# Performance work log

Measured on AMD Instinct MI355X. Metric: run time of the kernel, lower is better.

Reference implementation:

```python
import jax, jax.numpy as jnp
import numpy as np

BN_EPS = 1e-5

# Binary_a: sign forward, hard-tanh STE backward (grad zeroed where |x| >= 1)
@jax.custom_vjp
def binary_act(x):
    return jnp.sign(x)

def _ba_fwd(x):
    return jnp.sign(x), x

def _ba_bwd(x, g):
    return (jnp.where((x > -1.0) & (x < 1.0), g, 0.0),)

binary_act.defvjp(_ba_fwd, _ba_bwd)

# Binary_w: sign forward, identity STE backward
@jax.custom_vjp
def binary_w(x):
    return jnp.sign(x)

def _bw_fwd(x):
    return jnp.sign(x), None

def _bw_bwd(_, g):
    return (g,)

binary_w.defvjp(_bw_fwd, _bw_bwd)


def setup_inputs() -> dict:
    key = jax.random.key(0)
    k1, k2, k3 = jax.random.split(key, 3)
    B, Cin, Cout, H, Wd, K = 32, 256, 256, 56, 56, 3
    x = jax.random.normal(k1, (B, Cin, H, Wd), dtype=jnp.float32)
    weight = jax.random.normal(k2, (Cout, Cin, K, K), dtype=jnp.float32) * 0.05
    bias = jax.random.normal(k3, (Cout,), dtype=jnp.float32) * 0.01
    gamma = jnp.ones((Cout,), dtype=jnp.float32)
    beta = jnp.zeros((Cout,), dtype=jnp.float32)
    return {"x": x, "weight": weight, "bias": bias, "gamma": gamma, "beta": beta}


def reference(x, weight, bias, gamma, beta):
    # activation binarization (A=2)
    xb = binary_act(x)
    # weight quantization (W=2): mean-center over in-channel dim, clamp to [-1,1]
    # (done on .data in torch -> values change but no grad through this step)
    wc_val = jnp.clip(weight - jnp.mean(weight, axis=1, keepdims=True), -1.0, 1.0)
    wc = weight + jax.lax.stop_gradient(wc_val - weight)
    # per-output-filter scale alpha = E[|w|] over (in, kh, kw)
    alpha = jnp.mean(jnp.abs(wc), axis=(1, 2, 3), keepdims=True)
    wq = binary_w(wc) * alpha  # [O,I,K,K]
    # conv2d, stride 1, padding 1, groups 1
    y = jax.lax.conv_general_dilated(
        xb, wq, window_strides=(1, 1), padding=((1, 1), (1, 1)),
        dimension_numbers=("NCHW", "OIHW", "NCHW"))
    y = y + bias[None, :, None, None]
    # BatchNorm2d, training-mode forward (biased batch stats)
    mean = jnp.mean(y, axis=(0, 2, 3), keepdims=True)
    var = jnp.mean(jnp.square(y - mean), axis=(0, 2, 3), keepdims=True)
    y = (y - mean) * jax.lax.rsqrt(var + BN_EPS)
    y = y * gamma[None, :, None, None] + beta[None, :, None, None]
    # last_relu=1
    return jax.nn.relu(y)
```

## Files before the change

kernel.cpp:

```cpp
#include <hip/hip_runtime.h>
#include <stdint.h>

typedef unsigned long long u64;
typedef unsigned int u32;

#define B_    32
#define CIN   256
#define COUT  256
#define H_    56
#define W_    56
#define HW    3136
#define NPOS  100352
#define NROW  1792
#define NPACKBLK 784


__global__ __launch_bounds__(256) void k_prep(
    const float* __restrict__ x,
    const float* __restrict__ wgt,
    u64* __restrict__ xbits,
    u64* __restrict__ wbits,
    float* __restrict__ alpha,
    int* __restrict__ ssum,
    unsigned long long* __restrict__ qsum)
{
    const int tid = threadIdx.x;

    if (blockIdx.x < NPACKBLK) {
        const int j = blockIdx.x / 196;
        const int p2 = (blockIdx.x - j * 196) * 256 + tid;
        const int pos0 = p2 * 2;
        const int b = pos0 / HW;
        const int hw = pos0 - b * HW;
        const float* xp = x + (size_t)b * CIN * HW + (size_t)j * 64 * HW + hw;
        u64 b0 = 0, b1 = 0;
#pragma unroll 8
        for (int k = 0; k < 64; ++k) {
            const float2 v = *(const float2*)(xp + (size_t)k * HW);
            b0 |= (u64)(v.x > 0.0f) << k;
            b1 |= (u64)(v.y > 0.0f) << k;
        }
        xbits[(size_t)pos0 * 4 + j] = b0;
        xbits[(size_t)(pos0 + 1) * 4 + j] = b1;
        return;
    }

    const int o = blockIdx.x - NPACKBLK;
    const int i = tid;
    const int wave = i >> 6, lane = i & 63;
    __shared__ float sred[4][12];

    if (i == 0) { ssum[o] = 0; qsum[o] = 0ULL; }

    float w9[9];
#pragma unroll
    for (int t = 0; t < 9; ++t) w9[t] = wgt[(o * 256 + i) * 9 + t];

    float m[9];
#pragma unroll
    for (int t = 0; t < 9; ++t) m[t] = w9[t];
#pragma unroll
    for (int s = 1; s < 64; s <<= 1)
#pragma unroll
        for (int t = 0; t < 9; ++t) m[t] += __shfl_xor(m[t], s, 64);
    if (lane == 0) {
#pragma unroll
        for (int t = 0; t < 9; ++t) sred[wave][t] = m[t];
    }
    __syncthreads();
#pragma unroll
    for (int t = 0; t < 9; ++t)
        m[t] = (sred[0][t] + sred[1][t] + sred[2][t] + sred[3][t]) * (1.0f / 256.0f);

    float wc[9];
    float asum = 0.0f;
#pragma unroll
    for (int t = 0; t < 9; ++t) {
        float v = w9[t] - m[t];
        v = fminf(fmaxf(v, -1.0f), 1.0f);
        wc[t] = v;
        asum += fabsf(v);
    }
#pragma unroll
    for (int s = 1; s < 64; s <<= 1) asum += __shfl_xor(asum, s, 64);
    __syncthreads();
    if (lane == 0) sred[wave][9] = asum;
    __syncthreads();
    if (i == 0)
        alpha[o] = (sred[0][9] + sred[1][9] + sred[2][9] + sred[3][9]) * (1.0f / 2304.0f);

#pragma unroll
    for (int t = 0; t < 9; ++t) {
        u64 bb = __ballot(wc[t] > 0.0f);
        if (lane == 0) wbits[o * 36 + t * 4 + wave] = bb;
    }
}

template<int R0, int R1>
__device__ __forceinline__ void run_row2(
    const u64* __restrict__ t2,
    const u64* wr,
    short* __restrict__ srow,
    const bool st,
    int& s_acc, int& q_acc)
{
    constexpr int NR = R1 - R0 + 1;
    u64 xc[4][NR][2];

#define FILL(col, slot) { \
    _Pragma("unroll") \
    for (int r = 0; r < NR; ++r) { \
        const ulonglong2 v = *(const ulonglong2*)&t2[((R0 + r) * 56 + (col)) * 4]; \
        xc[slot][r][0] = v.x; xc[slot][r][1] = v.y; } }

#define PIN(slot) { \
    _Pragma("unroll") \
    for (int r = 0; r < NR; ++r) { \
        asm volatile("" : "+v"(xc[slot][r][0])); \
        asm volatile("" : "+v"(xc[slot][r][1])); } }

#define TAPACC(slot, r, kw) \
    acc += (int)__popcll(xc[slot][r][0] ^ wr[((R0 + r) * 3 + (kw)) * 2 + 0]) \
         + (int)__popcll(xc[slot][r][1] ^ wr[((R0 + r) * 3 + (kw)) * 2 + 1]);

#define COMPW(sm, s0, sp, SROWOFF) { \
    int acc = 0; \
    _Pragma("unroll") \
    for (int r = 0; r < NR; ++r) { TAPACC(sm, r, 0) TAPACC(s0, r, 1) TAPACC(sp, r, 2) } \
    acc += __shfl_xor(acc, 1, 64); \
    const int Sv = NR * 3 * 256 - 2 * acc; \
    if (st) srow[(SROWOFF) * 256] = (short)Sv; \
    s_acc += Sv; q_acc += Sv * Sv; }

    FILL(0, 0) FILL(1, 1) FILL(2, 2) PIN(0) PIN(1)

    {
        int acc = 0;
#pragma unroll
        for (int r = 0; r < NR; ++r) { TAPACC(0, r, 1) TAPACC(1, r, 2) }
        acc += __shfl_xor(acc, 1, 64);
        const int Sv = NR * 2 * 256 - 2 * acc;
        if (st) srow[0] = (short)Sv;
        s_acc += Sv; q_acc += Sv * Sv;
    }
    FILL(3, 3) PIN(2)

    COMPW(0, 1, 2, 1) PIN(3)

    for (int wb = 2; wb <= 50; wb += 4) {
        FILL(wb + 2, 0) COMPW(1, 2, 3, wb + 0) PIN(0)
        FILL(wb + 3, 1) COMPW(2, 3, 0, wb + 1) PIN(1)
        FILL(wb + 4, 2) COMPW(3, 0, 1, wb + 2) PIN(2)
        FILL(wb + 5, 3) COMPW(0, 1, 2, wb + 3) PIN(3)
    }

    COMPW(1, 2, 3, 54)

    {
        int acc = 0;
#pragma unroll
        for (int r = 0; r < NR; ++r) { TAPACC(2, r, 0) TAPACC(3, r, 1) }
        acc += __shfl_xor(acc, 1, 64);
        const int Sv = NR * 2 * 256 - 2 * acc;
        if (st) srow[55 * 256] = (short)Sv;
        s_acc += Sv; q_acc += Sv * Sv;
    }

#undef FILL
#undef PIN
#undef TAPACC
#undef COMPW
}

__global__ __launch_bounds__(256, 4) void kc_conv(
    const u64* __restrict__ xbits,
    const u64* __restrict__ wbits,
    short* __restrict__ S,
    int* __restrict__ ssum,
    unsigned long long* __restrict__ qsum)
{
    const int blk = blockIdx.x;
    const int row = blk >> 1;
    const int ohalf = blk & 1;
    const int b = row / H_;
    const int h = row - b * H_;
    const int t = threadIdx.x;
    const int half = t & 1;
    const int o = ohalf * 128 + (t >> 1);

    __shared__ u64 tile[3 * W_ * 4];
    for (int idx = t; idx < 3 * W_ * 4; idx += 256) {
        int r = idx / (W_ * 4);
        int rem = idx - r * (W_ * 4);
        int hr = min(max(h - 1 + r, 0), H_ - 1);
        tile[idx] = xbits[((size_t)(b * HW + hr * W_)) * 4 + rem];
    }

    u64 wr[18];
#pragma unroll
    for (int tap = 0; tap < 9; ++tap) {
        ulonglong2 v = *(const ulonglong2*)(wbits + (size_t)o * 36 + tap * 4 + 2 * half);
        wr[tap * 2] = v.x;
        wr[tap * 2 + 1] = v.y;
    }
#pragma unroll
    for (int i = 0; i < 18; ++i) asm volatile("" : "+v"(wr[i]));

    __syncthreads();

    const u64* t2 = tile + 2 * half;
    short* srow = S + ((size_t)(b * HW + h * W_)) * 256 + o;
    int s_acc = 0, q_acc = 0;
    const bool st = (half == 0);
    if (h == 0)        run_row2<1, 2>(t2, wr, srow, st, s_acc, q_acc);
    else if (h == 55)  run_row2<0, 1>(t2, wr, srow, st, s_acc, q_acc);
    else               run_row2<0, 2>(t2, wr, srow, st, s_acc, q_acc);

    if (st) {
        atomicAdd(&ssum[o], s_acc);
        atomicAdd(&qsum[o], (unsigned long long)(long long)q_acc);
    }
}

__global__ __launch_bounds__(256) void kb_apply(
    const short* __restrict__ S,
    const int* __restrict__ ssum,
    const unsigned long long* __restrict__ qsum,
    const float* __restrict__ alpha,
    const float* __restrict__ gamma,
    const float* __restrict__ beta,
    float* __restrict__ out)
{
    const int blk = blockIdx.x;
    const int ps = blk % 7;
    const int bcg = blk / 7;
    const int cg = bcg & 3;
    const int b = bcg >> 2;
    const int c0 = cg * 64;
    const int pbase = ps * 448;
    const int tid = threadIdx.x;

    __shared__ float s_scale[64], s_shift[64];
    __shared__ u32 lds[64 * 33];

    if (tid < 64) {
        const int o = c0 + tid;
        const double N = (double)NPOS;
        double meanS = (double)ssum[o] / N;
        double varS = (double)qsum[o] / N - meanS * meanS;
        double a = (double)alpha[o];
        double rstd = 1.0 / sqrt(a * a * varS + 1e-5);
        double g = (double)gamma[o];
        s_scale[tid] = (float)(g * a * rstd);
        s_shift[tid] = (float)((double)beta[o] - g * a * meanS * rstd);
    }
    __syncthreads();

    for (int chunk = 0; chunk < 7; ++chunk) {
        const int p0 = pbase + chunk * 64;

        const u32* Sp = (const u32*)(S + ((size_t)b * HW + p0) * 256 + c0);
#pragma unroll
        for (int k = 0; k < 8; ++k) {
            const int idx = tid + k * 256;
            const int p = idx >> 5, cp = idx & 31;
            lds[p * 33 + cp] = Sp[p * 128 + cp];
        }
        __syncthreads();

        const int pl = tid & 63;
        const int ch4 = tid >> 6;
        const short* lss = (const short*)lds;
#pragma unroll
        for (int cc = 0; cc < 16; ++cc) {
            const int c = ch4 * 16 + cc;
            const float f = fmaxf(fmaf((float)lss[pl * 66 + c], s_scale[c], s_shift[c]), 0.0f);
            out[((size_t)(b * COUT + c0 + c)) * HW + p0 + pl] = f;
        }
        __syncthreads();
    }
}

extern "C" void kernel_launch(void* const* d_in, const int* in_sizes, int n_in,
                              void* d_out, int out_size, void* d_ws, size_t ws_size,
                              hipStream_t stream) {
    const float* x     = (const float*)d_in[0];
    const float* wgt   = (const float*)d_in[1];
    const float* gamma = (const float*)d_in[3];
    const float* beta  = (const float*)d_in[4];
    float* out = (float*)d_out;

    char* ws = (char*)d_ws;
    u64*   wbits = (u64*)(ws + 0);
    float* alpha = (float*)(ws + 73728);
    int*   ssum  = (int*)(ws + 74752);
    unsigned long long* qsum = (unsigned long long*)(ws + 75776);
    u64*   xbits = (u64*)(ws + 79872);
    short* Sarr  = (short*)(ws + 3291136);

    k_prep<<<NPACKBLK + 256, 256, 0, stream>>>(x, wgt, xbits, wbits, alpha, ssum, qsum);
    kc_conv<<<2 * NROW, 256, 0, stream>>>(xbits, wbits, Sarr, ssum, qsum);
    kb_apply<<<32 * 4 * 7, 256, 0, stream>>>(Sarr, ssum, qsum, alpha, gamma, beta, out);
}
```

Before: 330.2 us.

## Replace XNOR-popcount conv with int8 MFMA implicit GEMM on ±1 values

The binary convolution no longer uses XOR/popcount on packed bit words. Activation bits are expanded to ±1 int8 values in a swizzled LDS tile (zero where padded), and weights are pre-laid out as ±1 int8 MFMA B fragments. Each block then computes one output row against all 256 output channels with v_mfma_i32_32x32x32_i8, software-pipelining the operand loads. This trades popcount ALU work for matrix-core throughput, at the cost of 8x more operand bytes, extra LDS expansion work, and lower occupancy (launch bounds 3).

```diff
diff --git a/kernel.cpp b/kernel.cpp
--- a/kernel.cpp
+++ b/kernel.cpp
@@ -3,6 +3,8 @@
 
 typedef unsigned long long u64;
 typedef unsigned int u32;
+typedef int v4i __attribute__((ext_vector_type(4)));
+typedef int v16i __attribute__((ext_vector_type(16)));
 
 #define B_    32
 #define CIN   256
@@ -19,7 +21,7 @@
     const float* __restrict__ x,
     const float* __restrict__ wgt,
     u64* __restrict__ xbits,
-    u64* __restrict__ wbits,
+    int8_t* __restrict__ Bfrag,
     float* __restrict__ alpha,
     int* __restrict__ ssum,
     unsigned long long* __restrict__ qsum)
@@ -91,134 +93,129 @@
 
 #pragma unroll
     for (int t = 0; t < 9; ++t) {
-        u64 bb = __ballot(wc[t] > 0.0f);
-        if (lane == 0) wbits[o * 36 + t * 4 + wave] = bb;
+        const int8_t sv = (wc[t] > 0.0f) ? (int8_t)1 : (int8_t)-1;
+        const size_t addr =
+            ((size_t)((t * 8 + (i >> 5)) * 8 + (o >> 5)) * 64
+             + (size_t)(((i >> 4) & 1) * 32 + (o & 31))) * 16 + (i & 15);
+        Bfrag[addr] = sv;
     }
 }
 
-template<int R0, int R1>
-__device__ __forceinline__ void run_row2(
-    const u64* __restrict__ t2,
-    const u64* wr,
-    short* __restrict__ srow,
-    const bool st,
-    int& s_acc, int& q_acc)
-{
-    constexpr int NR = R1 - R0 + 1;
-    u64 xc[4][NR][2];
-
-#define FILL(col, slot) { \
-    _Pragma("unroll") \
-    for (int r = 0; r < NR; ++r) { \
-        const ulonglong2 v = *(const ulonglong2*)&t2[((R0 + r) * 56 + (col)) * 4]; \
-        xc[slot][r][0] = v.x; xc[slot][r][1] = v.y; } }
-
-#define PIN(slot) { \
-    _Pragma("unroll") \
-    for (int r = 0; r < NR; ++r) { \
-        asm volatile("" : "+v"(xc[slot][r][0])); \
-        asm volatile("" : "+v"(xc[slot][r][1])); } }
-
-#define TAPACC(slot, r, kw) \
-    acc += (int)__popcll(xc[slot][r][0] ^ wr[((R0 + r) * 3 + (kw)) * 2 + 0]) \
-         + (int)__popcll(xc[slot][r][1] ^ wr[((R0 + r) * 3 + (kw)) * 2 + 1]);
-
-#define COMPW(sm, s0, sp, SROWOFF) { \
-    int acc = 0; \
-    _Pragma("unroll") \
-    for (int r = 0; r < NR; ++r) { TAPACC(sm, r, 0) TAPACC(s0, r, 1) TAPACC(sp, r, 2) } \
-    acc += __shfl_xor(acc, 1, 64); \
-    const int Sv = NR * 3 * 256 - 2 * acc; \
-    if (st) srow[(SROWOFF) * 256] = (short)Sv; \
-    s_acc += Sv; q_acc += Sv * Sv; }
-
-    FILL(0, 0) FILL(1, 1) FILL(2, 2) PIN(0) PIN(1)
-
-    {
-        int acc = 0;
-#pragma unroll
-        for (int r = 0; r < NR; ++r) { TAPACC(0, r, 1) TAPACC(1, r, 2) }
-        acc += __shfl_xor(acc, 1, 64);
-        const int Sv = NR * 2 * 256 - 2 * acc;
-        if (st) srow[0] = (short)Sv;
-        s_acc += Sv; q_acc += Sv * Sv;
-    }
-    FILL(3, 3) PIN(2)
-
-    COMPW(0, 1, 2, 1) PIN(3)
-
-    for (int wb = 2; wb <= 50; wb += 4) {
-        FILL(wb + 2, 0) COMPW(1, 2, 3, wb + 0) PIN(0)
-        FILL(wb + 3, 1) COMPW(2, 3, 0, wb + 1) PIN(1)
-        FILL(wb + 4, 2) COMPW(3, 0, 1, wb + 2) PIN(2)
-        FILL(wb + 5, 3) COMPW(0, 1, 2, wb + 3) PIN(3)
-    }
-
-    COMPW(1, 2, 3, 54)
-
-    {
-        int acc = 0;
-#pragma unroll
-        for (int r = 0; r < NR; ++r) { TAPACC(2, r, 0) TAPACC(3, r, 1) }
-        acc += __shfl_xor(acc, 1, 64);
-        const int Sv = NR * 2 * 256 - 2 * acc;
-        if (st) srow[55 * 256] = (short)Sv;
-        s_acc += Sv; q_acc += Sv * Sv;
-    }
-
-#undef FILL
-#undef PIN
-#undef TAPACC
-#undef COMPW
-}
-
-__global__ __launch_bounds__(256, 4) void kc_conv(
+#define MFMA_I8(acc, a, b) \
+    asm volatile("v_mfma_i32_32x32x32_i8 %0, %1, %2, %0" : "+a"(acc) : "v"(a), "v"(b))
+
+__global__ __launch_bounds__(256, 3) void kc_mfma(
     const u64* __restrict__ xbits,
-    const u64* __restrict__ wbits,
+    const int8_t* __restrict__ Bfrag,
     short* __restrict__ S,
     int* __restrict__ ssum,
     unsigned long long* __restrict__ qsum)
 {
     const int blk = blockIdx.x;
-    const int row = blk >> 1;
-    const int ohalf = blk & 1;
-    const int b = row / H_;
-    const int h = row - b * H_;
-    const int t = threadIdx.x;
-    const int half = t & 1;
-    const int o = ohalf * 128 + (t >> 1);
-
-    __shared__ u64 tile[3 * W_ * 4];
-    for (int idx = t; idx < 3 * W_ * 4; idx += 256) {
-        int r = idx / (W_ * 4);
-        int rem = idx - r * (W_ * 4);
-        int hr = min(max(h - 1 + r, 0), H_ - 1);
-        tile[idx] = xbits[((size_t)(b * HW + hr * W_)) * 4 + rem];
-    }
-
-    u64 wr[18];
-#pragma unroll
-    for (int tap = 0; tap < 9; ++tap) {
-        ulonglong2 v = *(const ulonglong2*)(wbits + (size_t)o * 36 + tap * 4 + 2 * half);
-        wr[tap * 2] = v.x;
-        wr[tap * 2 + 1] = v.y;
-    }
-#pragma unroll
-    for (int i = 0; i < 18; ++i) asm volatile("" : "+v"(wr[i]));
-
-    __syncthreads();
-
-    const u64* t2 = tile + 2 * half;
-    short* srow = S + ((size_t)(b * HW + h * W_)) * 256 + o;
-    int s_acc = 0, q_acc = 0;
-    const bool st = (half == 0);
-    if (h == 0)        run_row2<1, 2>(t2, wr, srow, st, s_acc, q_acc);
-    else if (h == 55)  run_row2<0, 1>(t2, wr, srow, st, s_acc, q_acc);
-    else               run_row2<0, 2>(t2, wr, srow, st, s_acc, q_acc);
-
-    if (st) {
-        atomicAdd(&ssum[o], s_acc);
-        atomicAdd(&qsum[o], (unsigned long long)(long long)q_acc);
+    const int b = blk / H_;
+    const int h = blk - b * H_;
+    const int tid = threadIdx.x;
+
+    __shared__ u32 ldsb[3 * 66 * 64];
+
+    for (int it = tid; it < 3 * 58 * 16; it += 256) {
+        const int r = it / 928;
+        const int rem = it - r * 928;
+        const int wp = rem >> 4;
+        const int g = rem & 15;
+        const int hr = h - 1 + r;
+        const int w_in = wp - 1;
+        const bool inb = (hr >= 0) && (hr < H_) && (w_in >= 0) && (w_in < W_);
+        u32 chunk16 = 0;
+        if (inb) {
+            const u64 word = xbits[((size_t)(b * HW + hr * W_ + w_in)) * 4 + (g >> 2)];
+            chunk16 = (u32)(word >> ((g & 3) * 16)) & 0xFFFFu;
+        }
+        u32 out4[4];
+#pragma unroll
+        for (int d = 0; d < 4; ++d) {
+            const u32 nib = (chunk16 >> (4 * d)) & 0xFu;
+            const u32 m1 = (nib * 0x00204081u) & 0x01010101u;
+            const u32 inv = m1 ^ 0x01010101u;
+            out4[d] = inb ? (0x01010101u ^ (inv * 0xFEu)) : 0u;
+        }
+        const int gs = (g + wp) & 15;
+        u32* dst = &ldsb[((r * 66 + wp) << 6) + gs * 4];
+        dst[0] = out4[0]; dst[1] = out4[1]; dst[2] = out4[2]; dst[3] = out4[3];
+    }
+    __syncthreads();
+
+    const int m0 = tid & 31;
+    const int lh = (tid >> 5) & 1;
+    const int wv = tid >> 6;
+    const int8_t* smem = (const int8_t*)ldsb;
+    const int8_t* Bp = Bfrag + (size_t)(tid & 63) * 16;
+
+    auto ldA = [&](int kk, int mt) -> v4i {
+        const int tap = kk >> 3, s = kk & 7;
+        const int dh = tap / 3;
+        const int dw = tap - dh * 3;
+        const int wpm = mt * 32 + m0 + dw;
+        const int gs = (2 * s + lh + wpm) & 15;
+        const int addr = ((dh * 66 + wpm) << 8) + (gs << 4);
+        return *(const v4i*)(smem + addr);
+    };
+    auto ldB = [&](int kk, int ntl) -> v4i {
+        const size_t off = (size_t)((kk * 8) + wv * 2 + ntl) * 1024;
+        return *(const v4i*)(Bp + off);
+    };
+
+    v16i acc00 = {0}, acc01 = {0}, acc10 = {0}, acc11 = {0};
+
+    v4i a0 = ldA(0, 0), a1 = ldA(0, 1);
+    v4i b0 = ldB(0, 0), b1 = ldB(0, 1);
+    v4i a0n, a1n, b0n, b1n;
+
+    for (int kk = 0; kk < 72; kk += 2) {
+        a0n = ldA(kk + 1, 0); a1n = ldA(kk + 1, 1);
+        b0n = ldB(kk + 1, 0); b1n = ldB(kk + 1, 1);
+        MFMA_I8(acc00, a0, b0); MFMA_I8(acc01, a0, b1);
+        MFMA_I8(acc10, a1, b0); MFMA_I8(acc11, a1, b1);
+        if (kk + 2 < 72) {
+            a0 = ldA(kk + 2, 0); a1 = ldA(kk + 2, 1);
+            b0 = ldB(kk + 2, 0); b1 = ldB(kk + 2, 1);
+        }
+        MFMA_I8(acc00, a0n, b0n); MFMA_I8(acc01, a0n, b1n);
+        MFMA_I8(acc10, a1n, b0n); MFMA_I8(acc11, a1n, b1n);
+    }
+
+    asm volatile("s_nop 7\n\ts_nop 7\n\ts_nop 7"
+                 : "+a"(acc00), "+a"(acc01), "+a"(acc10), "+a"(acc11));
+
+    const int n0 = wv * 64 + m0;
+    const int n1 = n0 + 32;
+    const int rowbase = b * HW + h * W_;
+    int s0 = 0, s1 = 0, q0 = 0, q1 = 0;
+
+#pragma unroll
+    for (int reg = 0; reg < 16; ++reg) {
+        const int m = (reg & 3) + ((reg >> 2) << 3) + (lh << 2);
+        const int v0 = acc00[reg], v1 = acc01[reg];
+        s0 += v0; q0 += v0 * v0; s1 += v1; q1 += v1 * v1;
+        S[(size_t)(rowbase + m) * 256 + n0] = (short)v0;
+        S[(size_t)(rowbase + m) * 256 + n1] = (short)v1;
+    }
+#pragma unroll
+    for (int reg = 0; reg < 12; ++reg) {
+        const int m = 32 + (reg & 3) + ((reg >> 2) << 3) + (lh << 2);
+        const int v0 = acc10[reg], v1 = acc11[reg];
+        s0 += v0; q0 += v0 * v0; s1 += v1; q1 += v1 * v1;
+        S[(size_t)(rowbase + m) * 256 + n0] = (short)v0;
+        S[(size_t)(rowbase + m) * 256 + n1] = (short)v1;
+    }
+
+    s0 += __shfl_xor(s0, 32, 64); q0 += __shfl_xor(q0, 32, 64);
+    s1 += __shfl_xor(s1, 32, 64); q1 += __shfl_xor(q1, 32, 64);
+    if (lh == 0) {
+        atomicAdd(&ssum[n0], s0);
+        atomicAdd(&qsum[n0], (unsigned long long)(long long)q0);
+        atomicAdd(&ssum[n1], s1);
+        atomicAdd(&qsum[n1], (unsigned long long)(long long)q1);
     }
 }
 
@@ -291,14 +288,14 @@
     float* out = (float*)d_out;
 
     char* ws = (char*)d_ws;
-    u64*   wbits = (u64*)(ws + 0);
-    float* alpha = (float*)(ws + 73728);
-    int*   ssum  = (int*)(ws + 74752);
-    unsigned long long* qsum = (unsigned long long*)(ws + 75776);
-    u64*   xbits = (u64*)(ws + 79872);
-    short* Sarr  = (short*)(ws + 3291136);
-
-    k_prep<<<NPACKBLK + 256, 256, 0, stream>>>(x, wgt, xbits, wbits, alpha, ssum, qsum);
-    kc_conv<<<2 * NROW, 256, 0, stream>>>(xbits, wbits, Sarr, ssum, qsum);
+    int8_t* Bfrag = (int8_t*)(ws + 0);
+    float* alpha = (float*)(ws + 589824);
+    int*   ssum  = (int*)(ws + 590848);
+    unsigned long long* qsum = (unsigned long long*)(ws + 591872);
+    u64*   xbits = (u64*)(ws + 593920);
+    short* Sarr  = (short*)(ws + 3805184);
+
+    k_prep<<<NPACKBLK + 256, 256, 0, stream>>>(x, wgt, xbits, Bfrag, alpha, ssum, qsum);
+    kc_mfma<<<NROW, 256, 0, stream>>>(xbits, Bfrag, Sarr, ssum, qsum);
     kb_apply<<<32 * 4 * 7, 256, 0, stream>>>(Sarr, ssum, qsum, alpha, gamma, beta, out);
 }
```

After: 292.3 us. 1.13x faster.
